# Kernel tuning notes

Measured on AMD Instinct MI355X. Metric: run time of the kernel, lower is better.

The kernel has to match this reference:

```python
import jax, jax.numpy as jnp
import numpy as np

N = 1_000_000
KNN = 9
C_IN = 20      # in_channel
C_INNER = 20   # inner_channel
REPEAT = 2
EPS = 1e-5


def _bn(x, gamma, beta, axes):
    # training-mode batchnorm over given axes, per-channel (last axis) affine
    mean = jnp.mean(x, axis=axes, keepdims=True)
    var = jnp.var(x, axis=axes, keepdims=True)
    return (x - mean) * jax.lax.rsqrt(var + EPS) * gamma + beta


def setup_inputs() -> dict:
    key = jax.random.key(0)
    ks = jax.random.split(key, 12)
    s = lambda fan: 1.0 / np.sqrt(fan)
    return {
        "points": jax.random.normal(ks[0], (N, 3), jnp.float32),
        "feature": jax.random.normal(ks[1], (N, C_INNER), jnp.float32),
        "index": jax.random.randint(ks[2], (N, KNN), 0, N, jnp.int64),
        # conv2: Conv1d(inner+3 -> inner, k=1, no bias) + BN
        "W1": jax.random.normal(ks[3], (C_INNER, C_INNER + 3), jnp.float32) * s(C_INNER + 3),
        "g1": jnp.ones((C_INNER,), jnp.float32),
        "b1": jnp.zeros((C_INNER,), jnp.float32),
        # bn_relu
        "g2": jnp.ones((C_INNER,), jnp.float32),
        "b2": jnp.zeros((C_INNER,), jnp.float32),
        # refine: Linear(in+inner -> in) + BN + ReLU + Linear(in -> in)
        "Wr1": jax.random.normal(ks[4], (C_IN, C_IN + C_INNER), jnp.float32) * s(C_IN + C_INNER),
        "br1": jnp.zeros((C_IN,), jnp.float32),
        "g3": jnp.ones((C_IN,), jnp.float32),
        "b3": jnp.zeros((C_IN,), jnp.float32),
        "Wr2": jax.random.normal(ks[5], (C_IN, C_IN), jnp.float32) * s(C_IN),
        "br2": jnp.zeros((C_IN,), jnp.float32),
    }


def reference(points, feature, index, W1, g1, b1, g2, b2, Wr1, br1, g3, b3, Wr2, br2):
    # gather neighbor coords, center on each point: [N, K, 3]
    xyz = points[index] - points[:, None, :]
    # gather neighbor features and concat: [N, K, C_inner+3]
    x = jnp.concatenate([feature[index], xyz], axis=-1)
    # 1x1 conv == per-(point,neighbor) linear, then BN over (N, K)
    x = jnp.einsum('nkc,oc->nko', x, W1)
    x = _bn(x, g1, b1, (0, 1))                      # [N, K, C_inner]
    # attention weight: dot of each neighbor with neighbor 0, over channels
    w = jnp.sum(x * x[:, :1, :], axis=-1)           # [N, K]
    # (original computes softmax(w) but never uses it; faithful: use raw w)
    x = jnp.sum(x * w[:, :, None], axis=1)          # [N, C_inner]
    for _ in range(REPEAT - 1):
        x = jnp.sum(x[index] * w[:, :, None], axis=1)
    x = jax.nn.relu(_bn(x, g2, b2, (0,)))
    x = jnp.concatenate([x, feature], axis=-1)      # [N, C_in + C_inner]
    x = jax.nn.relu(_bn(x @ Wr1.T + br1, g3, b3, (0,)))
    return x @ Wr2.T + br2                          # [N, C_in]
```

## Files before the change

### kernel.cpp

```cpp
#include <hip/hip_runtime.h>
#include <hip/hip_fp16.h>


constexpr int KNN_ = 9;
constexpr int CI   = 20;
constexpr int CC   = 23;
constexpr int CAT  = 40;
constexpr int USH  = 32;
constexpr float EPS = 1e-5f;

template <int CNT>
__device__ __forceinline__ void block_reduce_add(float (&v)[CNT], double* __restrict__ dst,
                                                 float* __restrict__ lds ) {
    const int lane = threadIdx.x & 63;
    const int wid  = threadIdx.x >> 6;
#pragma unroll
    for (int i = 0; i < CNT; ++i) {
        float x = v[i];
#pragma unroll
        for (int off = 32; off > 0; off >>= 1) x += __shfl_down(x, off);
        if (lane == 0) lds[wid * CNT + i] = x;
    }
    __syncthreads();
    if (threadIdx.x < CNT) {
        float x = lds[threadIdx.x] + lds[CNT + threadIdx.x] +
                  lds[2 * CNT + threadIdx.x] + lds[3 * CNT + threadIdx.x];
        atomicAdd(dst + threadIdx.x, (double)x);
    }
}

__device__ __forceinline__ void loadrow20(const float* __restrict__ p, float (&v)[CI]) {
    const float4* q = reinterpret_cast<const float4*>(p);
    const float4 a = q[0], b = q[1], c = q[2], d = q[3], e = q[4];
    v[0]=a.x; v[1]=a.y; v[2]=a.z; v[3]=a.w;
    v[4]=b.x; v[5]=b.y; v[6]=b.z; v[7]=b.w;
    v[8]=c.x; v[9]=c.y; v[10]=c.z; v[11]=c.w;
    v[12]=d.x; v[13]=d.y; v[14]=d.z; v[15]=d.w;
    v[16]=e.x; v[17]=e.y; v[18]=e.z; v[19]=e.w;
}

__device__ __forceinline__ void storerow20(float* __restrict__ p, const float (&v)[CI]) {
    float4* q = reinterpret_cast<float4*>(p);
    q[0] = make_float4(v[0],  v[1],  v[2],  v[3]);
    q[1] = make_float4(v[4],  v[5],  v[6],  v[7]);
    q[2] = make_float4(v[8],  v[9],  v[10], v[11]);
    q[3] = make_float4(v[12], v[13], v[14], v[15]);
    q[4] = make_float4(v[16], v[17], v[18], v[19]);
}

__device__ __forceinline__ float2 h2f(unsigned int u) {
    return __half22float2(__builtin_bit_cast(__half2, u));
}

__device__ __forceinline__ void loadrow20h(const __half* __restrict__ p, float (&v)[CI]) {
    const uint4 A = reinterpret_cast<const uint4*>(p)[0];
    const uint4 B = reinterpret_cast<const uint4*>(p)[1];
    const uint2 C = reinterpret_cast<const uint2*>(p)[4];
    float2 f;
    f = h2f(A.x); v[0]=f.x;  v[1]=f.y;
    f = h2f(A.y); v[2]=f.x;  v[3]=f.y;
    f = h2f(A.z); v[4]=f.x;  v[5]=f.y;
    f = h2f(A.w); v[6]=f.x;  v[7]=f.y;
    f = h2f(B.x); v[8]=f.x;  v[9]=f.y;
    f = h2f(B.y); v[10]=f.x; v[11]=f.y;
    f = h2f(B.z); v[12]=f.x; v[13]=f.y;
    f = h2f(B.w); v[14]=f.x; v[15]=f.y;
    f = h2f(C.x); v[16]=f.x; v[17]=f.y;
    f = h2f(C.y); v[18]=f.x; v[19]=f.y;
}

__device__ __forceinline__ unsigned int f2h(float a, float b) {
    return __builtin_bit_cast(unsigned int, __float22half2_rn(make_float2(a, b)));
}

__device__ __forceinline__ void storerow20h(__half* __restrict__ p, const float (&v)[CI]) {
    uint4* q = reinterpret_cast<uint4*>(p);
    q[0] = make_uint4(f2h(v[0],v[1]),   f2h(v[2],v[3]),   f2h(v[4],v[5]),   f2h(v[6],v[7]));
    q[1] = make_uint4(f2h(v[8],v[9]),   f2h(v[10],v[11]), f2h(v[12],v[13]), f2h(v[14],v[15]));
    q[2] = make_uint4(f2h(v[16],v[17]), f2h(v[18],v[19]), 0u, 0u);
    q[3] = make_uint4(0u, 0u, 0u, 0u);
}

__global__ __launch_bounds__(256) void k0_uv(
    const float* __restrict__ points, const float* __restrict__ feature,
    const float* __restrict__ W1, __half* __restrict__ u, int N)
{
    __shared__ float Ws[CI * CC];
    for (int i = threadIdx.x; i < CI * CC; i += 256) Ws[i] = W1[i];
    __syncthreads();
    const int n = blockIdx.x * 256 + threadIdx.x;
    if (n >= N) return;
    float in[CI];
    loadrow20(feature + (size_t)n * CI, in);
    const float px = points[3*n], py = points[3*n+1], pz = points[3*n+2];
    float uo[CI];
#pragma unroll
    for (int o = 0; o < CI; ++o) {
        float y = Ws[o*CC+20] * px;
        y = fmaf(Ws[o*CC+21], py, y);
        y = fmaf(Ws[o*CC+22], pz, y);
#pragma unroll
        for (int c = 0; c < CI; ++c) y = fmaf(Ws[o*CC+c], in[c], y);
        uo[o] = y;
    }
    storerow20h(u + (size_t)n * USH, uo);
}

__global__ __launch_bounds__(256, 3) void k1_stats(
    const float* __restrict__ points, const int* __restrict__ index,
    const float* __restrict__ W1, const __half* __restrict__ u,
    double* __restrict__ stats, int N)
{
    __shared__ float Ws[CI * CC];
    __shared__ float red[4 * 2 * CI];
    for (int i = threadIdx.x; i < CI * CC; i += 256) Ws[i] = W1[i];
    __syncthreads();

    float acc[2 * CI];
#pragma unroll
    for (int i = 0; i < 2 * CI; ++i) acc[i] = 0.f;

#pragma unroll 1
    for (int n = blockIdx.x * 256 + threadIdx.x; n < N; n += gridDim.x * 256) {
        const float px = points[3*n], py = points[3*n+1], pz = points[3*n+2];
        float v[CI];
#pragma unroll
        for (int o = 0; o < CI; ++o) {
            float t = Ws[o*CC+20] * px;
            t = fmaf(Ws[o*CC+21], py, t);
            v[o] = fmaf(Ws[o*CC+22], pz, t);
        }
        int idx[KNN_];
#pragma unroll
        for (int k = 0; k < KNN_; ++k) idx[k] = index[n * KNN_ + k];

#pragma unroll 1
        for (int t = 0; t < 4; ++t) {
            float ra[CI], rb[CI];
            loadrow20h(u + (size_t)idx[2*t]   * USH, ra);
            loadrow20h(u + (size_t)idx[2*t+1] * USH, rb);
#pragma unroll
            for (int o = 0; o < CI; ++o) {
                const float d = ra[o] - v[o];
                acc[o] += d;
                acc[CI + o] = fmaf(d, d, acc[CI + o]);
            }
#pragma unroll
            for (int o = 0; o < CI; ++o) {
                const float d = rb[o] - v[o];
                acc[o] += d;
                acc[CI + o] = fmaf(d, d, acc[CI + o]);
            }
        }
        {
            float ra[CI];
            loadrow20h(u + (size_t)idx[8] * USH, ra);
#pragma unroll
            for (int o = 0; o < CI; ++o) {
                const float d = ra[o] - v[o];
                acc[o] += d;
                acc[CI + o] = fmaf(d, d, acc[CI + o]);
            }
        }
    }
    __syncthreads();
    block_reduce_add<2 * CI>(acc, stats, red);
}

__global__ __launch_bounds__(256, 3) void k3_attn(
    const float* __restrict__ points, const int* __restrict__ index,
    const float* __restrict__ W1, const float* __restrict__ g1,
    const float* __restrict__ b1, const double* __restrict__ stats,
    const __half* __restrict__ u,
    float* __restrict__ wbuf, __half* __restrict__ xagg, int N)
{
    __shared__ float Ws[CI * CC];
    __shared__ float sc[CI], sh[CI];
    for (int i = threadIdx.x; i < CI * CC; i += 256) Ws[i] = W1[i];
    if (threadIdx.x < CI) {
        const double M = (double)N * KNN_;
        const double mean = stats[threadIdx.x] / M;
        const double var  = stats[CI + threadIdx.x] / M - mean * mean;
        const float s = g1[threadIdx.x] * rsqrtf((float)var + EPS);
        sc[threadIdx.x] = s;
        sh[threadIdx.x] = b1[threadIdx.x] - (float)mean * s;
    }
    __syncthreads();

    const int n = blockIdx.x * 256 + threadIdx.x;
    if (n >= N) return;

    const float px = points[3*n], py = points[3*n+1], pz = points[3*n+2];
    float v2[CI];
#pragma unroll
    for (int o = 0; o < CI; ++o) {
        float t = Ws[o*CC+20] * px;
        t = fmaf(Ws[o*CC+21], py, t);
        t = fmaf(Ws[o*CC+22], pz, t);
        v2[o] = fmaf(t, sc[o], -sh[o]);
    }
    int idx[KNN_];
#pragma unroll
    for (int k = 0; k < KNN_; ++k) idx[k] = index[n * KNN_ + k];

    float x0[CI], accv[CI];
    {
        float r[CI];
        loadrow20h(u + (size_t)idx[0] * USH, r);
        float w0 = 0.f;
#pragma unroll
        for (int o = 0; o < CI; ++o) x0[o] = fmaf(r[o], sc[o], -v2[o]);
#pragma unroll
        for (int o = 0; o < CI; ++o) w0 = fmaf(x0[o], x0[o], w0);
        wbuf[n * KNN_] = w0;
#pragma unroll
        for (int o = 0; o < CI; ++o) accv[o] = x0[o] * w0;
    }
#pragma unroll 1
    for (int t = 0; t < 4; ++t) {
        const int ka = 1 + 2*t, kb = 2 + 2*t;
        float ra[CI], rb[CI];
        loadrow20h(u + (size_t)idx[ka] * USH, ra);
        loadrow20h(u + (size_t)idx[kb] * USH, rb);
        float wa = 0.f, wb = 0.f;
#pragma unroll
        for (int o = 0; o < CI; ++o) {
            ra[o] = fmaf(ra[o], sc[o], -v2[o]);
            wa = fmaf(ra[o], x0[o], wa);
        }
#pragma unroll
        for (int o = 0; o < CI; ++o) {
            rb[o] = fmaf(rb[o], sc[o], -v2[o]);
            wb = fmaf(rb[o], x0[o], wb);
        }
        wbuf[n * KNN_ + ka] = wa;
        wbuf[n * KNN_ + kb] = wb;
#pragma unroll
        for (int o = 0; o < CI; ++o) accv[o] = fmaf(ra[o], wa, accv[o]);
#pragma unroll
        for (int o = 0; o < CI; ++o) accv[o] = fmaf(rb[o], wb, accv[o]);
    }
    storerow20h(xagg + (size_t)n * USH, accv);
}

__global__ __launch_bounds__(256, 3) void k4_prop(
    const int* __restrict__ index, const float* __restrict__ wbuf,
    const __half* __restrict__ xagg, float* __restrict__ x2,
    double* __restrict__ stats2, int N)
{
    __shared__ float red[4 * 2 * CI];
    float st[2 * CI];
#pragma unroll
    for (int i = 0; i < 2 * CI; ++i) st[i] = 0.f;

#pragma unroll 1
    for (int n = blockIdx.x * 256 + threadIdx.x; n < N; n += gridDim.x * 256) {
        int idx[KNN_];
        float wk[KNN_];
#pragma unroll
        for (int k = 0; k < KNN_; ++k) idx[k] = index[n * KNN_ + k];
#pragma unroll
        for (int k = 0; k < KNN_; ++k) wk[k] = wbuf[n * KNN_ + k];

        float accv[CI];
        {
            float r[CI];
            loadrow20h(xagg + (size_t)idx[0] * USH, r);
#pragma unroll
            for (int o = 0; o < CI; ++o) accv[o] = r[o] * wk[0];
        }
#pragma unroll 1
        for (int t = 0; t < 4; ++t) {
            const int ka = 1 + 2*t, kb = 2 + 2*t;
            float ra[CI], rb[CI];
            loadrow20h(xagg + (size_t)idx[ka] * USH, ra);
            loadrow20h(xagg + (size_t)idx[kb] * USH, rb);
#pragma unroll
            for (int o = 0; o < CI; ++o) accv[o] = fmaf(ra[o], wk[ka], accv[o]);
#pragma unroll
            for (int o = 0; o < CI; ++o) accv[o] = fmaf(rb[o], wk[kb], accv[o]);
        }
        storerow20(x2 + (size_t)n * CI, accv);
#pragma unroll
        for (int o = 0; o < CI; ++o) {
            st[o] += accv[o];
            st[CI + o] = fmaf(accv[o], accv[o], st[CI + o]);
        }
    }
    __syncthreads();
    block_reduce_add<2 * CI>(st, stats2, red);
}

__global__ __launch_bounds__(256) void k6_refine1(
    const float* __restrict__ x2, const float* __restrict__ feature,
    const float* __restrict__ g2, const float* __restrict__ b2,
    const float* __restrict__ Wr1, const float* __restrict__ br1,
    const double* __restrict__ stats2,
    float* __restrict__ ybuf, int N)
{
    __shared__ float Ws[CI * CAT];
    __shared__ float sc[CI], sh[CI], brs[CI];
    for (int i = threadIdx.x; i < CI * CAT; i += 256) Ws[i] = Wr1[i];
    if (threadIdx.x < CI) {
        const double M = (double)N;
        const double mean = stats2[threadIdx.x] / M;
        const double var  = stats2[CI + threadIdx.x] / M - mean * mean;
        const float s = g2[threadIdx.x] * rsqrtf((float)var + EPS);
        sc[threadIdx.x] = s;
        sh[threadIdx.x] = b2[threadIdx.x] - (float)mean * s;
        brs[threadIdx.x] = br1[threadIdx.x];
    }
    __syncthreads();

    const int n = blockIdx.x * 256 + threadIdx.x;
    if (n >= N) return;

    float in[CI];
    loadrow20(x2 + (size_t)n * CI, in);
#pragma unroll
    for (int o = 0; o < CI; ++o)
        in[o] = fmaxf(fmaf(in[o], sc[o], sh[o]), 0.f);
    float yv[CI];
#pragma unroll
    for (int o = 0; o < CI; ++o) {
        float y = brs[o];
#pragma unroll
        for (int c = 0; c < CI; ++c) y = fmaf(Ws[o * CAT + c], in[c], y);
        yv[o] = y;
    }
    loadrow20(feature + (size_t)n * CI, in);
#pragma unroll
    for (int o = 0; o < CI; ++o) {
        float y = yv[o];
#pragma unroll
        for (int c = 0; c < CI; ++c) y = fmaf(Ws[o * CAT + CI + c], in[c], y);
        yv[o] = y;
    }
    storerow20(ybuf + (size_t)n * CI, yv);
}

__global__ __launch_bounds__(256) void k7_stats3(
    const float* __restrict__ ybuf, double* __restrict__ stats3, int N)
{
    __shared__ float red[4 * 2 * CI];
    float st[2 * CI];
#pragma unroll
    for (int i = 0; i < 2 * CI; ++i) st[i] = 0.f;

#pragma unroll 1
    for (int n = blockIdx.x * 256 + threadIdx.x; n < N; n += gridDim.x * 256) {
        float yv[CI];
        loadrow20(ybuf + (size_t)n * CI, yv);
#pragma unroll
        for (int o = 0; o < CI; ++o) {
            st[o] += yv[o];
            st[CI + o] = fmaf(yv[o], yv[o], st[CI + o]);
        }
    }
    __syncthreads();
    block_reduce_add<2 * CI>(st, stats3, red);
}

__global__ __launch_bounds__(256) void k8_out(
    const float* __restrict__ ybuf,
    const float* __restrict__ g3, const float* __restrict__ b3,
    const float* __restrict__ Wr2, const float* __restrict__ br2,
    const double* __restrict__ stats3, float* __restrict__ out, int N)
{
    __shared__ float Ws[CI * CI];
    __shared__ float sc[CI], sh[CI];
    for (int i = threadIdx.x; i < CI * CI; i += 256) Ws[i] = Wr2[i];
    if (threadIdx.x < CI) {
        const double M = (double)N;
        const double mean = stats3[threadIdx.x] / M;
        const double var  = stats3[CI + threadIdx.x] / M - mean * mean;
        const float s = g3[threadIdx.x] * rsqrtf((float)var + EPS);
        sc[threadIdx.x] = s;
        sh[threadIdx.x] = b3[threadIdx.x] - (float)mean * s;
    }
    __syncthreads();

    const int n = blockIdx.x * 256 + threadIdx.x;
    if (n >= N) return;

    float z[CI];
    {
        float yi[CI];
        loadrow20(ybuf + (size_t)n * CI, yi);
#pragma unroll
        for (int o = 0; o < CI; ++o)
            z[o] = fmaxf(fmaf(yi[o], sc[o], sh[o]), 0.f);
    }
    float ov[CI];
#pragma unroll
    for (int o = 0; o < CI; ++o) {
        float y = br2[o];
#pragma unroll
        for (int c = 0; c < CI; ++c) y = fmaf(Ws[o * CI + c], z[c], y);
        ov[o] = y;
    }
    storerow20(out + (size_t)n * CI, ov);
}

extern "C" void kernel_launch(void* const* d_in, const int* in_sizes, int n_in,
                              void* d_out, int out_size, void* d_ws, size_t ws_size,
                              hipStream_t stream) {
    const float* points  = (const float*)d_in[0];
    const float* feature = (const float*)d_in[1];
    const int*   index   = (const int*)  d_in[2];
    const float* W1      = (const float*)d_in[3];
    const float* g1      = (const float*)d_in[4];
    const float* b1      = (const float*)d_in[5];
    const float* g2      = (const float*)d_in[6];
    const float* b2      = (const float*)d_in[7];
    const float* Wr1     = (const float*)d_in[8];
    const float* br1     = (const float*)d_in[9];
    const float* g3      = (const float*)d_in[10];
    const float* b3      = (const float*)d_in[11];
    const float* Wr2     = (const float*)d_in[12];
    const float* br2     = (const float*)d_in[13];
    const int N = in_sizes[0] / 3;
    float* out = (float*)d_out;

    double* stats = (double*)d_ws;
    char* base = (char*)d_ws;
    size_t off = 1024;
    float*  wbuf = (float*)(base + off); off += (size_t)N * KNN_ * 4;
    __half* u    = (__half*)(base + off);
    float*  x2   = (float*)(base + off); off += (size_t)N * CI * 4;
    __half* xagg = (__half*)(base + off);
    float*  ybuf = (float*)(base + off);

    hipMemsetAsync(stats, 0, 6 * CI * sizeof(double), stream);

    const int B = 256;
    const int gridN = (N + B - 1) / B;
    k0_uv     <<<gridN, B, 0, stream>>>(points, feature, W1, u, N);
    k1_stats  <<<2048, B, 0, stream>>>(points, index, W1, u, stats, N);
    k3_attn   <<<gridN, B, 0, stream>>>(points, index, W1, g1, b1, stats, u, wbuf, xagg, N);
    k4_prop   <<<2048, B, 0, stream>>>(index, wbuf, xagg, x2, stats + 2 * CI, N);
    k6_refine1<<<gridN, B, 0, stream>>>(x2, feature, g2, b2, Wr1, br1, stats + 2 * CI, ybuf, N);
    k7_stats3 <<<2048, B, 0, stream>>>(ybuf, stats + 4 * CI, N);
    k8_out    <<<gridN, B, 0, stream>>>(ybuf, g3, b3, Wr2, br2, stats + 4 * CI, out, N);
}
```

Baseline: 949.2 us.

## Replace neighbor-gather BN statistics with scatter-accumulated point sums and moments

Batchnorm statistics for the first conv are rewritten algebraically: instead of gathering nine neighbor feature rows per point, each point's coordinates and a count are atomically scattered to its neighbors, then a streaming pass over u combines these with per-point moments. Mean and variance are reconstructed in k3_attn from the sum, square, and cross terms plus global coordinate moments. This removes random 9x gathers of u but adds 36 random float atomics per point and an extra buffer memset, with possible precision differences from cancellation.

New measurement: 2.619 ms. 2.76x slower.

```diff
diff --git a/kernel.cpp b/kernel.cpp
--- a/kernel.cpp
+++ b/kernel.cpp
@@ -106,65 +106,72 @@
     storerow20h(u + (size_t)n * USH, uo);
 }
 
-__global__ __launch_bounds__(256, 3) void k1_stats(
+__global__ __launch_bounds__(256, 3) void k1a_scatter(
     const float* __restrict__ points, const int* __restrict__ index,
-    const float* __restrict__ W1, const __half* __restrict__ u,
-    double* __restrict__ stats, int N)
-{
-    __shared__ float Ws[CI * CC];
-    __shared__ float red[4 * 2 * CI];
-    for (int i = threadIdx.x; i < CI * CC; i += 256) Ws[i] = W1[i];
-    __syncthreads();
-
-    float acc[2 * CI];
-#pragma unroll
-    for (int i = 0; i < 2 * CI; ++i) acc[i] = 0.f;
+    float* __restrict__ qc, double* __restrict__ stats, int N)
+{
+    __shared__ float red[4 * 9];
+    float accP[9];
+#pragma unroll
+    for (int i = 0; i < 9; ++i) accP[i] = 0.f;
 
 #pragma unroll 1
     for (int n = blockIdx.x * 256 + threadIdx.x; n < N; n += gridDim.x * 256) {
         const float px = points[3*n], py = points[3*n+1], pz = points[3*n+2];
-        float v[CI];
+        accP[0] += px; accP[1] += py; accP[2] += pz;
+        accP[3] = fmaf(px, px, accP[3]);
+        accP[4] = fmaf(px, py, accP[4]);
+        accP[5] = fmaf(px, pz, accP[5]);
+        accP[6] = fmaf(py, py, accP[6]);
+        accP[7] = fmaf(py, pz, accP[7]);
+        accP[8] = fmaf(pz, pz, accP[8]);
+        int idx[KNN_];
+#pragma unroll
+        for (int k = 0; k < KNN_; ++k) idx[k] = index[n * KNN_ + k];
+#pragma unroll
+        for (int k = 0; k < KNN_; ++k) {
+            float* qj = qc + 4 * (size_t)idx[k];
+            atomicAdd(qj + 0, px);
+            atomicAdd(qj + 1, py);
+            atomicAdd(qj + 2, pz);
+            atomicAdd(qj + 3, 1.0f);
+        }
+    }
+    __syncthreads();
+    block_reduce_add<9>(accP, stats + 60, red);
+}
+
+__global__ __launch_bounds__(256, 3) void k1b_reduce(
+    const __half* __restrict__ u, const float* __restrict__ qc,
+    const float* __restrict__ W1, double* __restrict__ stats, int N)
+{
+    __shared__ float Ws[CI * CC];
+    __shared__ float red[4 * 3 * CI];
+    for (int i = threadIdx.x; i < CI * CC; i += 256) Ws[i] = W1[i];
+    __syncthreads();
+
+    float acc[3 * CI];
+#pragma unroll
+    for (int i = 0; i < 3 * CI; ++i) acc[i] = 0.f;
+
+#pragma unroll 1
+    for (int n = blockIdx.x * 256 + threadIdx.x; n < N; n += gridDim.x * 256) {
+        float uo[CI];
+        loadrow20h(u + (size_t)n * USH, uo);
+        const float4 q = reinterpret_cast<const float4*>(qc)[n];
 #pragma unroll
         for (int o = 0; o < CI; ++o) {
-            float t = Ws[o*CC+20] * px;
-            t = fmaf(Ws[o*CC+21], py, t);
-            v[o] = fmaf(Ws[o*CC+22], pz, t);
-        }
-        int idx[KNN_];
-#pragma unroll
-        for (int k = 0; k < KNN_; ++k) idx[k] = index[n * KNN_ + k];
-
-#pragma unroll 1
-        for (int t = 0; t < 4; ++t) {
-            float ra[CI], rb[CI];
-            loadrow20h(u + (size_t)idx[2*t]   * USH, ra);
-            loadrow20h(u + (size_t)idx[2*t+1] * USH, rb);
-#pragma unroll
-            for (int o = 0; o < CI; ++o) {
-                const float d = ra[o] - v[o];
-                acc[o] += d;
-                acc[CI + o] = fmaf(d, d, acc[CI + o]);
-            }
-#pragma unroll
-            for (int o = 0; o < CI; ++o) {
-                const float d = rb[o] - v[o];
-                acc[o] += d;
-                acc[CI + o] = fmaf(d, d, acc[CI + o]);
-            }
-        }
-        {
-            float ra[CI];
-            loadrow20h(u + (size_t)idx[8] * USH, ra);
-#pragma unroll
-            for (int o = 0; o < CI; ++o) {
-                const float d = ra[o] - v[o];
-                acc[o] += d;
-                acc[CI + o] = fmaf(d, d, acc[CI + o]);
-            }
-        }
-    }
-    __syncthreads();
-    block_reduce_add<2 * CI>(acc, stats, red);
+            const float cu = q.w * uo[o];
+            acc[o] += cu;
+            acc[CI + o] = fmaf(cu, uo[o], acc[CI + o]);
+            float r = Ws[o*CC+20] * q.x;
+            r = fmaf(Ws[o*CC+21], q.y, r);
+            r = fmaf(Ws[o*CC+22], q.z, r);
+            acc[2*CI + o] = fmaf(uo[o], r, acc[2*CI + o]);
+        }
+    }
+    __syncthreads();
+    block_reduce_add<3 * CI>(acc, stats, red);
 }
 
 __global__ __launch_bounds__(256, 3) void k3_attn(
@@ -178,12 +185,22 @@
     __shared__ float sc[CI], sh[CI];
     for (int i = threadIdx.x; i < CI * CC; i += 256) Ws[i] = W1[i];
     if (threadIdx.x < CI) {
-        const double M = (double)N * KNN_;
-        const double mean = stats[threadIdx.x] / M;
-        const double var  = stats[CI + threadIdx.x] / M - mean * mean;
-        const float s = g1[threadIdx.x] * rsqrtf((float)var + EPS);
-        sc[threadIdx.x] = s;
-        sh[threadIdx.x] = b1[threadIdx.x] - (float)mean * s;
+        const int o = threadIdx.x;
+        const double A = stats[o], B = stats[CI + o], C = stats[2*CI + o];
+        const double P1x = stats[60], P1y = stats[61], P1z = stats[62];
+        const double xx = stats[63], xy = stats[64], xz = stats[65];
+        const double yy = stats[66], yz = stats[67], zz = stats[68];
+        const double w0 = W1[o*CC+20], w1 = W1[o*CC+21], w2 = W1[o*CC+22];
+        const double Sv  = w0*P1x + w1*P1y + w2*P1z;
+        const double Svv = w0*w0*xx + w1*w1*yy + w2*w2*zz
+                         + 2.0*(w0*w1*xy + w0*w2*xz + w1*w2*yz);
+        const double M9 = (double)N * KNN_;
+        const double mean = (A - (double)KNN_ * Sv) / M9;
+        const double Ey2  = (B - 2.0*C + (double)KNN_ * Svv) / M9;
+        const double var  = Ey2 - mean * mean;
+        const float s = g1[o] * rsqrtf((float)var + EPS);
+        sc[o] = s;
+        sh[o] = b1[o] - (float)mean * s;
     }
     __syncthreads();
 
@@ -424,22 +441,25 @@
 
     double* stats = (double*)d_ws;
     char* base = (char*)d_ws;
-    size_t off = 1024;
+    size_t off = 2048;
     float*  wbuf = (float*)(base + off); off += (size_t)N * KNN_ * 4;
     __half* u    = (__half*)(base + off);
     float*  x2   = (float*)(base + off); off += (size_t)N * CI * 4;
     __half* xagg = (__half*)(base + off);
-    float*  ybuf = (float*)(base + off);
-
-    hipMemsetAsync(stats, 0, 6 * CI * sizeof(double), stream);
+    float*  ybuf = (float*)(base + off); off += (size_t)N * CI * 4;
+    float*  qc   = (float*)(base + off);
+
+    hipMemsetAsync(stats, 0, 160 * sizeof(double), stream);
+    hipMemsetAsync(qc, 0, (size_t)N * 4 * sizeof(float), stream);
 
     const int B = 256;
     const int gridN = (N + B - 1) / B;
-    k0_uv     <<<gridN, B, 0, stream>>>(points, feature, W1, u, N);
-    k1_stats  <<<2048, B, 0, stream>>>(points, index, W1, u, stats, N);
-    k3_attn   <<<gridN, B, 0, stream>>>(points, index, W1, g1, b1, stats, u, wbuf, xagg, N);
-    k4_prop   <<<2048, B, 0, stream>>>(index, wbuf, xagg, x2, stats + 2 * CI, N);
-    k6_refine1<<<gridN, B, 0, stream>>>(x2, feature, g2, b2, Wr1, br1, stats + 2 * CI, ybuf, N);
-    k7_stats3 <<<2048, B, 0, stream>>>(ybuf, stats + 4 * CI, N);
-    k8_out    <<<gridN, B, 0, stream>>>(ybuf, g3, b3, Wr2, br2, stats + 4 * CI, out, N);
-}
+    k0_uv      <<<gridN, B, 0, stream>>>(points, feature, W1, u, N);
+    k1a_scatter<<<2048, B, 0, stream>>>(points, index, qc, stats, N);
+    k1b_reduce <<<2048, B, 0, stream>>>(u, qc, W1, stats, N);
+    k3_attn    <<<gridN, B, 0, stream>>>(points, index, W1, g1, b1, stats, u, wbuf, xagg, N);
+    k4_prop    <<<2048, B, 0, stream>>>(index, wbuf, xagg, x2, stats + 80, N);
+    k6_refine1 <<<gridN, B, 0, stream>>>(x2, feature, g2, b2, Wr1, br1, stats + 80, ybuf, N);
+    k7_stats3  <<<2048, B, 0, stream>>>(ybuf, stats + 120, N);
+    k8_out     <<<gridN, B, 0, stream>>>(ybuf, g3, b3, Wr2, br2, stats + 120, out, N);
+}
```
